# Optimization experiments

Measured on AMD Instinct MI355X. Metric: run time of the kernel, lower is better.

Reference implementation:

```python
import jax, jax.numpy as jnp
import numpy as np
import math

BN_EPS = 1e-5
LOG20 = math.log(20.0)

def conv1x1(w, x):
    # w: [O, C], x: [B, C, N] -> [B, O, N]
    return jnp.einsum('oc,bcn->bon', w, x)

def bn_silu(x, g, b, m, v):
    # inference-mode BatchNorm1d over channel dim, then SiLU
    y = (x - m[None, :, None]) * (g / jnp.sqrt(v + BN_EPS))[None, :, None] + b[None, :, None]
    return y * jax.nn.sigmoid(y)

def setup_inputs() -> dict:
    key = jax.random.key(0)
    ks = jax.random.split(key, 16)
    B, N, M = 8, 4096, 4096
    f32 = jnp.float32
    d = {
        'pcd_f': jax.random.normal(ks[0], (B, 1152, N), f32),
        'img_f': jax.random.normal(ks[1], (B, 1024, M), f32),
        'q_w': jax.random.normal(ks[2], (1024, 1152), f32) * 0.02,
        'k_w': jax.random.normal(ks[3], (1024, 1024), f32) * 0.02,
        'v_w': jax.random.normal(ks[4], (1024, 1024), f32) * 0.02,
        'skip_w': jax.random.normal(ks[5], (1024, 1152), f32) * 0.02,
        'c1_w': jax.random.normal(ks[6], (256, 1024), f32) * 0.03,
        'bn1_g': jnp.ones((256,), f32),
        'bn1_b': jnp.zeros((256,), f32),
        'bn1_m': jax.random.normal(ks[7], (256,), f32) * 0.1,
        'bn1_v': jnp.ones((256,), f32) + 0.1 * jax.random.uniform(ks[8], (256,)),
        'c2_w': jax.random.normal(ks[9], (64, 256), f32) * 0.06,
        'bn2_g': jnp.ones((64,), f32),
        'bn2_b': jnp.zeros((64,), f32),
        'bn2_m': jax.random.normal(ks[10], (64,), f32) * 0.1,
        'bn2_v': jnp.ones((64,), f32) + 0.1 * jax.random.uniform(ks[11], (64,)),
        'c3_w': jax.random.normal(ks[12], (1, 64), f32) * 0.1,
        'c3_b': jnp.zeros((1,), f32),
    }
    return d

def reference(pcd_f, img_f, q_w, k_w, v_w, skip_w, c1_w, bn1_g, bn1_b, bn1_m, bn1_v,
              c2_w, bn2_g, bn2_b, bn2_m, bn2_v, c3_w, c3_b):
    q = conv1x1(q_w, pcd_f)                       # [B, 1024, N]
    k = conv1x1(k_w, img_f)                       # [B, 1024, M]
    v = conv1x1(v_w, img_f)                       # [B, 1024, M]
    scale = math.sqrt(q.shape[1])                 # sqrt(C) = 32
    energy = jnp.einsum('bcn,bcm->bnm', q, k) / scale
    attn = jax.nn.softmax(energy, axis=-1)        # [B, N, M]
    x = jnp.einsum('bnm,bcm->bcn', attn, v)       # [B, 1024, N]
    x = conv1x1(skip_w, pcd_f) + x
    x = bn_silu(conv1x1(c1_w, x), bn1_g, bn1_b, bn1_m, bn1_v)   # [B, 256, N]
    x = bn_silu(conv1x1(c2_w, x), bn2_g, bn2_b, bn2_m, bn2_v)   # [B, 64, N]
    x = conv1x1(c3_w, x) + c3_b[None, :, None]    # [B, 1, N]
    x = x[:, 0, :]                                # squeeze channel -> [B, N]
    return jax.nn.sigmoid(x * LOG20)              # 1/(1+20^-x)
```

## Files before the change

kernel.cpp:

```cpp
#include <hip/hip_runtime.h>

#define LOG20F 2.9957322735539909f
#define AS1 __attribute__((address_space(1)))
#define AS3 __attribute__((address_space(3)))

typedef __attribute__((ext_vector_type(4))) short short4v;
typedef __attribute__((ext_vector_type(8))) short short8;
typedef __attribute__((ext_vector_type(8))) __bf16 bf16x8;
typedef __attribute__((ext_vector_type(4))) float f32x4;

__device__ __forceinline__ short f2bf(float f) {
  unsigned u = __float_as_uint(f);
  u = u + 0x7fffu + ((u >> 16) & 1u);
  return (short)(u >> 16);
}
__device__ __forceinline__ float bf2f(short s) {
  return __uint_as_float(((unsigned)(unsigned short)s) << 16);
}

__device__ __forceinline__ void xcd_map(int& bx, int& by, int& bz) {
  int gx = gridDim.x, gy = gridDim.y;
  int nwg = gx * gy * (int)gridDim.z;
  int lin = bx + gx * (by + gy * bz);
  int q = nwg >> 3, r = nwg & 7;
  int xcd = lin & 7, idx = lin >> 3;
  int wg = (xcd < r ? xcd * (q + 1) : r * (q + 1) + (xcd - r) * q) + idx;
  int per_z = gx * gy;
  bz = wg / per_z;
  int rz = wg - bz * per_z;
  if ((gx & 3) == 0 && (gy & 3) == 0) {
    int nstx = gx >> 2;
    int st = rz >> 4, w = rz & 15;
    bx = ((st % nstx) << 2) + (w & 3);
    by = ((st / nstx) << 2) + (w >> 2);
  } else {
    bx = rz % gx;
    by = rz / gx;
  }
}

template <int EPI>
__global__ __launch_bounds__(512, 2) void gemm8(
    const short* __restrict__ A, const short* __restrict__ B,
    short* __restrict__ C, const short* __restrict__ addp,
    int K, int lda, int ldb, int ldc,
    long abatch, long bbatch, long cbatch, float scale)
{
  __shared__ __align__(16) short lA[2][256 * 64];
  __shared__ __align__(16) short lB[2][256 * 64];

  int bx = blockIdx.x, by = blockIdx.y, bz = blockIdx.z;
  xcd_map(bx, by, bz);

  const int tid = threadIdx.x;
  const int lane = tid & 63, wid = tid >> 6;
  const int wr = wid >> 2, wc = wid & 3;

  const long bm = (long)bx * 256, bn = (long)by * 256;
  const short* Ab = A + (long)bz * abatch + bm * lda;
  const short* Bb = B + (long)bz * bbatch + bn * ldb;

  f32x4 acc[8][4] = {};

  const int NKT = K >> 6;

  auto stageA = [&](int buf, int kt, int half) {
    int k0 = kt << 6;
#pragma unroll
    for (int i = 0; i < 2; ++i) {
      int idx = i * 512 + tid;
      int rl = idx >> 3, ch = idx & 7;
      int row = half * 128 + rl;
      int chs = ch ^ (row & 7);
      __builtin_amdgcn_global_load_lds(
          (const AS1 void*)(Ab + (long)row * lda + k0 + chs * 8),
          (AS3 void*)(&lA[buf][row * 64 + ch * 8]), 16, 0, 0);
    }
  };
  auto stageB = [&](int buf, int kt, int half) {
    int k0 = kt << 6;
#pragma unroll
    for (int i = 0; i < 2; ++i) {
      int idx = i * 512 + tid;
      int rl = idx >> 3, ch = idx & 7;
      int row = half * 128 + rl;
      int chs = ch ^ (row & 7);
      __builtin_amdgcn_global_load_lds(
          (const AS1 void*)(Bb + (long)row * ldb + k0 + chs * 8),
          (AS3 void*)(&lB[buf][row * 64 + ch * 8]), 16, 0, 0);
    }
  };

  const int rr = lane & 15, cl = lane >> 4;
  bf16x8 bfr[4][2], af[2][2];

  auto loadA = [&](int buf, int q) {
#pragma unroll
    for (int f = 0; f < 2; ++f) {
      int row = wr * 128 + q * 32 + f * 16 + rr;
#pragma unroll
      for (int kk = 0; kk < 2; ++kk) {
        int pch = (kk * 4 + cl) ^ (row & 7);
        af[f][kk] = *(const bf16x8*)&lA[buf][row * 64 + pch * 8];
      }
    }
  };
  auto loadB = [&](int buf) {
#pragma unroll
    for (int ni = 0; ni < 4; ++ni) {
      int row = wc * 64 + ni * 16 + rr;
#pragma unroll
      for (int kk = 0; kk < 2; ++kk) {
        int pch = (kk * 4 + cl) ^ (row & 7);
        bfr[ni][kk] = *(const bf16x8*)&lB[buf][row * 64 + pch * 8];
      }
    }
  };

#define BAR() __builtin_amdgcn_s_barrier()
#define LGKM0() asm volatile("s_waitcnt lgkmcnt(0)" ::: "memory")
#define MFMA_Q(q)                                                        \
  do {                                                                   \
    __builtin_amdgcn_s_setprio(1);                                       \
    _Pragma("unroll")                                                    \
    for (int f = 0; f < 2; ++f)                                          \
      _Pragma("unroll")                                                  \
      for (int ni = 0; ni < 4; ++ni)                                     \
        _Pragma("unroll")                                                \
        for (int kk = 0; kk < 2; ++kk)                                   \
          acc[(q) * 2 + f][ni] = __builtin_amdgcn_mfma_f32_16x16x32_bf16(\
              af[f][kk], bfr[ni][kk], acc[(q) * 2 + f][ni], 0, 0, 0);    \
    __builtin_amdgcn_s_setprio(0);                                       \
  } while (0)

  stageB(0, 0, 0); stageB(0, 0, 1);
  stageA(0, 0, 0); stageA(0, 0, 1);
  stageB(1, 1, 0); stageB(1, 1, 1);
  asm volatile("s_waitcnt vmcnt(4)" ::: "memory");
  BAR();

  for (int t2 = 0; t2 < NKT; t2 += 2) {
    const bool more = (t2 + 4 <= NKT);
    loadB(0); loadA(0, 0);
    stageA(1, t2 + 1, 0); stageA(1, t2 + 1, 1);
    BAR(); LGKM0(); MFMA_Q(0); BAR();
    loadA(0, 1);
    if (more) stageB(0, t2 + 2, 0);
    BAR(); LGKM0(); MFMA_Q(1); BAR();
    loadA(0, 2);
    if (more) stageB(0, t2 + 2, 1);
    BAR(); LGKM0(); MFMA_Q(2); BAR();
    loadA(0, 3);
    if (more) { asm volatile("s_waitcnt vmcnt(4)" ::: "memory"); }
    else      { asm volatile("s_waitcnt vmcnt(0)" ::: "memory"); }
    BAR(); LGKM0(); MFMA_Q(3); BAR();
    loadB(1); loadA(1, 0);
    if (more) stageA(0, t2 + 2, 0);
    BAR(); LGKM0(); MFMA_Q(0); BAR();
    loadA(1, 1);
    if (more) stageA(0, t2 + 2, 1);
    BAR(); LGKM0(); MFMA_Q(1); BAR();
    loadA(1, 2);
    if (more) stageB(1, t2 + 3, 0);
    BAR(); LGKM0(); MFMA_Q(2); BAR();
    loadA(1, 3);
    if (more) stageB(1, t2 + 3, 1);
    if (more) { asm volatile("s_waitcnt vmcnt(4)" ::: "memory"); }
    else      { asm volatile("s_waitcnt vmcnt(0)" ::: "memory"); }
    BAR(); LGKM0(); MFMA_Q(3); BAR();
  }
#undef BAR
#undef LGKM0
#undef MFMA_Q

#pragma unroll
  for (int mi = 0; mi < 8; ++mi) {
    long row0 = bm + wr * 128 + (mi >> 1) * 32 + (mi & 1) * 16 + (cl << 2);
#pragma unroll
    for (int ni = 0; ni < 4; ++ni) {
      long col = bn + wc * 64 + ni * 16 + rr;
#pragma unroll
      for (int r = 0; r < 4; ++r) {
        long off = (long)bz * cbatch + (row0 + r) * ldc + col;
        float v = acc[mi][ni][r] * scale;
        if constexpr (EPI == 1) v += bf2f(addp[off]);
        C[off] = f2bf(v);
      }
    }
  }
}

__device__ __forceinline__ int swz32(int row, int ch) {
  return row * 32 + ((ch ^ ((row >> 1) & 3)) << 3);
}

template <int BM, int BN, int WR, int WC, int EPI>
__global__ __launch_bounds__(WR * WC * 64, 4) void gemm_bt(
    const short* __restrict__ A, const short* __restrict__ B,
    short* __restrict__ C, const short* __restrict__ addp,
    const float* __restrict__ sc, const float* __restrict__ sh,
    int K, int lda, int ldb, int ldc,
    long abatch, long bbatch, long cbatch, float scale)
{
  constexpr int NTH = WR * WC * 64;
  constexpr int WM = BM / WR, WN = BN / WC;
  constexpr int MR = WM / 16, NR = WN / 16;
  constexpr int CA = (BM * 4) / NTH, CB = (BN * 4) / NTH;

  __shared__ __align__(16) short lA[2][BM * 32];
  __shared__ __align__(16) short lB[2][BN * 32];

  int bx = blockIdx.x, by = blockIdx.y, bz = blockIdx.z;
  xcd_map(bx, by, bz);

  const int tid = threadIdx.x;
  const int lane = tid & 63, wid = tid >> 6;
  const int wr = wid / WC, wc = wid % WC;

  const long bm = (long)bx * BM, bn = (long)by * BN;
  const short* Ab = A + (long)bz * abatch + bm * lda;
  const short* Bb = B + (long)bz * bbatch + bn * ldb;

  f32x4 acc[MR][NR] = {};

  auto stage = [&](int buf, int k0) {
#pragma unroll
    for (int i = 0; i < CA; ++i) {
      int idx = i * NTH + tid, row = idx >> 2, ch = idx & 3;
      int chs = ch ^ ((row >> 1) & 3);
      __builtin_amdgcn_global_load_lds(
          (const AS1 void*)(Ab + (long)row * lda + k0 + chs * 8),
          (AS3 void*)(&lA[buf][idx * 8]), 16, 0, 0);
    }
#pragma unroll
    for (int i = 0; i < CB; ++i) {
      int idx = i * NTH + tid, row = idx >> 2, ch = idx & 3;
      int chs = ch ^ ((row >> 1) & 3);
      __builtin_amdgcn_global_load_lds(
          (const AS1 void*)(Bb + (long)row * ldb + k0 + chs * 8),
          (AS3 void*)(&lB[buf][idx * 8]), 16, 0, 0);
    }
  };

  const int NT = K >> 5;
  stage(0, 0);
  __syncthreads();
  int cur = 0;
  for (int t = 0; t < NT; ++t) {
    if (t + 1 < NT) stage(cur ^ 1, (t + 1) << 5);
    const int ch = lane >> 4, rrow = lane & 15;
    bf16x8 af[MR], bfr[NR];
#pragma unroll
    for (int mi = 0; mi < MR; ++mi) {
      int row = wr * WM + mi * 16 + rrow;
      af[mi] = *(const bf16x8*)&lA[cur][swz32(row, ch)];
    }
#pragma unroll
    for (int ni = 0; ni < NR; ++ni) {
      int row = wc * WN + ni * 16 + rrow;
      bfr[ni] = *(const bf16x8*)&lB[cur][swz32(row, ch)];
    }
    __builtin_amdgcn_s_setprio(1);
#pragma unroll
    for (int mi = 0; mi < MR; ++mi)
#pragma unroll
      for (int ni = 0; ni < NR; ++ni)
        acc[mi][ni] = __builtin_amdgcn_mfma_f32_16x16x32_bf16(
            af[mi], bfr[ni], acc[mi][ni], 0, 0, 0);
    __builtin_amdgcn_s_setprio(0);
    __syncthreads();
    cur ^= 1;
  }

#pragma unroll
  for (int mi = 0; mi < MR; ++mi) {
    long row0 = bm + wr * WM + mi * 16 + ((lane >> 4) << 2);
#pragma unroll
    for (int ni = 0; ni < NR; ++ni) {
      long col = bn + wc * WN + ni * 16 + (lane & 15);
#pragma unroll
      for (int r = 0; r < 4; ++r) {
        long off = (long)bz * cbatch + (row0 + r) * ldc + col;
        float v = acc[mi][ni][r] * scale;
        if constexpr (EPI == 1) v += bf2f(addp[off]);
        if constexpr (EPI == 2) {
          float y = v * sc[col] + sh[col];
          v = y / (1.f + __expf(-y));
        }
        C[off] = f2bf(v);
      }
    }
  }
}

__global__ __launch_bounds__(256) void transpose_cvt(
    const float* __restrict__ in, short* __restrict__ out, int C, int N)
{
  __shared__ float tile[32][33];
  int n0 = blockIdx.x * 32, c0 = blockIdx.y * 32;
  long z = (long)blockIdx.z * C * N;
  int tx = threadIdx.x & 31, ty = threadIdx.x >> 5;
#pragma unroll
  for (int r = 0; r < 4; ++r) {
    int cc = ty + r * 8;
    tile[cc][tx] = in[z + (long)(c0 + cc) * N + n0 + tx];
  }
  __syncthreads();
#pragma unroll
  for (int r = 0; r < 4; ++r) {
    int nn = ty + r * 8;
    out[z + (long)(n0 + nn) * C + c0 + tx] = f2bf(tile[tx][nn]);
  }
}

__global__ __launch_bounds__(256) void cvt_bf16(
    const float* __restrict__ in, short* __restrict__ out, long n)
{
  long i = ((long)blockIdx.x * 256 + threadIdx.x) * 4;
  if (i >= n) return;
  const float* p = in + i;
  short4v s;
  s[0] = f2bf(p[0]); s[1] = f2bf(p[1]); s[2] = f2bf(p[2]); s[3] = f2bf(p[3]);
  *(short4v*)(out + i) = s;
}

__global__ void bn_prep(const float* g1, const float* b1, const float* m1, const float* v1,
                        const float* g2, const float* b2, const float* m2, const float* v2,
                        float* s1, float* t1, float* s2, float* t2)
{
  int i = threadIdx.x;
  if (i < 256) { float s = g1[i] * rsqrtf(v1[i] + 1e-5f); s1[i] = s; t1[i] = b1[i] - m1[i] * s; }
  if (i < 64)  { float s = g2[i] * rsqrtf(v2[i] + 1e-5f); s2[i] = s; t2[i] = b2[i] - m2[i] * s; }
}

__global__ __launch_bounds__(256) void softmax_row(short* __restrict__ a)
{
  __shared__ float rm[4], rs[4];
  long row = blockIdx.x;
  short* p = a + row * 4096;
  int tid = threadIdx.x;
  short8 v0 = *(short8*)(p + tid * 16);
  short8 v1 = *(short8*)(p + tid * 16 + 8);
  float f[16];
#pragma unroll
  for (int j = 0; j < 8; ++j) { f[j] = bf2f(v0[j]); f[8 + j] = bf2f(v1[j]); }
  float m = f[0];
#pragma unroll
  for (int j = 1; j < 16; ++j) m = fmaxf(m, f[j]);
  for (int o = 32; o > 0; o >>= 1) m = fmaxf(m, __shfl_xor(m, o));
  if ((tid & 63) == 0) rm[tid >> 6] = m;
  __syncthreads();
  m = fmaxf(fmaxf(rm[0], rm[1]), fmaxf(rm[2], rm[3]));
  float s = 0.f;
#pragma unroll
  for (int j = 0; j < 16; ++j) { f[j] = __expf(f[j] - m); s += f[j]; }
  for (int o = 32; o > 0; o >>= 1) s += __shfl_xor(s, o);
  if ((tid & 63) == 0) rs[tid >> 6] = s;
  __syncthreads();
  s = rs[0] + rs[1] + rs[2] + rs[3];
  float inv = 1.f / s;
#pragma unroll
  for (int j = 0; j < 8; ++j) { v0[j] = f2bf(f[j] * inv); v1[j] = f2bf(f[8 + j] * inv); }
  *(short8*)(p + tid * 16) = v0;
  *(short8*)(p + tid * 16 + 8) = v1;
}

__global__ __launch_bounds__(256) void c3_out(
    const short* __restrict__ y2, const float* __restrict__ w,
    const float* __restrict__ bias, float* __restrict__ o, int total)
{
  int i = blockIdx.x * 256 + threadIdx.x;
  if (i >= total) return;
  const short8* r = (const short8*)(y2 + (long)i * 64);
  float acc = 0.f;
#pragma unroll
  for (int j0 = 0; j0 < 8; ++j0) {
    short8 v = r[j0];
#pragma unroll
    for (int j = 0; j < 8; ++j) acc += bf2f(v[j]) * w[j0 * 8 + j];
  }
  acc += bias[0];
  float x = acc * LOG20F;
  o[i] = 1.f / (1.f + __expf(-x));
}

extern "C" void kernel_launch(void* const* d_in, const int* in_sizes, int n_in,
                              void* d_out, int out_size, void* d_ws, size_t ws_size,
                              hipStream_t stream) {
  const float* pcd  = (const float*)d_in[0];
  const float* img  = (const float*)d_in[1];
  const float* qw   = (const float*)d_in[2];
  const float* kw   = (const float*)d_in[3];
  const float* vw   = (const float*)d_in[4];
  const float* skw  = (const float*)d_in[5];
  const float* c1w  = (const float*)d_in[6];
  const float* bn1g = (const float*)d_in[7];
  const float* bn1b = (const float*)d_in[8];
  const float* bn1m = (const float*)d_in[9];
  const float* bn1v = (const float*)d_in[10];
  const float* c2w  = (const float*)d_in[11];
  const float* bn2g = (const float*)d_in[12];
  const float* bn2b = (const float*)d_in[13];
  const float* bn2m = (const float*)d_in[14];
  const float* bn2v = (const float*)d_in[15];
  const float* c3w  = (const float*)d_in[16];
  const float* c3b  = (const float*)d_in[17];
  float* out = (float*)d_out;

  char* ws = (char*)d_ws;
  const long QS = 4096L * 1024;
  const long ES = 4096L * 4096;
  const size_t ALGN = 256;
  auto align_up = [&](size_t x) { return (x + ALGN - 1) & ~(ALGN - 1); };

  size_t oPcd = 0;
  size_t oImg = align_up(oPcd + 8L * 4096 * 1152 * 2);
  size_t oQt  = align_up(oImg + 8L * 4096 * 1024 * 2);
  size_t oKt  = align_up(oQt  + 8L * QS * 2);
  size_t oV   = align_up(oKt  + 8L * QS * 2);
  size_t oSk  = align_up(oV   + 8L * QS * 2);
  size_t oW   = align_up(oSk  + 8L * QS * 2);
  size_t oWq  = oW;
  size_t oWk  = align_up(oWq + 1024L * 1152 * 2);
  size_t oWv  = align_up(oWk + 1024L * 1024 * 2);
  size_t oWs  = align_up(oWv + 1024L * 1024 * 2);
  size_t oC1  = align_up(oWs + 1024L * 1152 * 2);
  size_t oC2  = align_up(oC1 + 256L * 1024 * 2);
  size_t oS1  = align_up(oC2 + 64L * 256 * 2);
  size_t oT1  = align_up(oS1 + 256 * 4);
  size_t oS2  = align_up(oT1 + 256 * 4);
  size_t oT2  = align_up(oS2 + 64 * 4);
  size_t oEnd = align_up(oT2 + 64 * 4);

  short* pcdT  = (short*)(ws + oPcd);
  short* imgT  = (short*)(ws + oImg);
  short* qt    = (short*)(ws + oQt);
  short* kt    = (short*)(ws + oKt);
  short* vbuf  = (short*)(ws + oV);
  short* skipT = (short*)(ws + oSk);
  short* wqb   = (short*)(ws + oWq);
  short* wkb   = (short*)(ws + oWk);
  short* wvb   = (short*)(ws + oWv);
  short* wskb  = (short*)(ws + oWs);
  short* c1b   = (short*)(ws + oC1);
  short* c2b   = (short*)(ws + oC2);
  float* s1 = (float*)(ws + oS1); float* t1 = (float*)(ws + oT1);
  float* s2 = (float*)(ws + oS2); float* t2 = (float*)(ws + oT2);

  int NB; short *attn, *xt;
  if (ws_size >= oEnd + (size_t)(4L * ES * 2)) {
    NB = 4; attn = (short*)(ws + 0); xt = (short*)(ws + oEnd);
  } else {
    NB = 2; attn = imgT; xt = pcdT;
  }
  short* y1t = qt;
  short* y2t = kt;

  cvt_bf16<<<dim3(1152), 256, 0, stream>>>(qw,  wqb,  1024L * 1152);
  cvt_bf16<<<dim3(1024), 256, 0, stream>>>(kw,  wkb,  1024L * 1024);
  cvt_bf16<<<dim3(1024), 256, 0, stream>>>(vw,  wvb,  1024L * 1024);
  cvt_bf16<<<dim3(1152), 256, 0, stream>>>(skw, wskb, 1024L * 1152);
  cvt_bf16<<<dim3(256),  256, 0, stream>>>(c1w, c1b,  256L * 1024);
  cvt_bf16<<<dim3(16),   256, 0, stream>>>(c2w, c2b,  64L * 256);
  bn_prep<<<1, 256, 0, stream>>>(bn1g, bn1b, bn1m, bn1v, bn2g, bn2b, bn2m, bn2v,
                                 s1, t1, s2, t2);
  transpose_cvt<<<dim3(128, 36, 8), 256, 0, stream>>>(pcd, pcdT, 1152, 4096);
  transpose_cvt<<<dim3(128, 32, 8), 256, 0, stream>>>(img, imgT, 1024, 4096);

  gemm8<0><<<dim3(16, 4, 8), 512, 0, stream>>>(
      pcdT, wqb, qt, nullptr, 1152, 1152, 1152, 1024, 4096L * 1152, 0, QS, 1.f);
  gemm8<0><<<dim3(16, 4, 8), 512, 0, stream>>>(
      imgT, wkb, kt, nullptr, 1024, 1024, 1024, 1024, QS, 0, QS, 1.f);
  gemm8<0><<<dim3(4, 16, 8), 512, 0, stream>>>(
      wvb, imgT, vbuf, nullptr, 1024, 1024, 1024, 4096, 0, QS, QS, 1.f);
  gemm8<0><<<dim3(16, 4, 8), 512, 0, stream>>>(
      pcdT, wskb, skipT, nullptr, 1152, 1152, 1152, 1024, 4096L * 1152, 0, QS, 1.f);

  for (int b0 = 0; b0 < 8; b0 += NB) {
    gemm8<0><<<dim3(16, 16, NB), 512, 0, stream>>>(
        qt + (long)b0 * QS, kt + (long)b0 * QS, attn, nullptr,
        1024, 1024, 1024, 4096, QS, QS, ES, 0.03125f);
    softmax_row<<<dim3(4096 * NB), 256, 0, stream>>>(attn);
    gemm8<1><<<dim3(16, 4, NB), 512, 0, stream>>>(
        attn, vbuf + (long)b0 * QS, xt + (long)b0 * QS, skipT + (long)b0 * QS,
        4096, 4096, 4096, 1024, ES, QS, QS, 1.f);
  }

  gemm_bt<128, 128, 2, 2, 2><<<dim3(32, 2, 8), 256, 0, stream>>>(
      xt, c1b, y1t, nullptr, s1, t1,
      1024, 1024, 1024, 256, QS, 0, 4096L * 256, 1.f);
  gemm_bt<128, 64, 4, 1, 2><<<dim3(32, 1, 8), 256, 0, stream>>>(
      y1t, c2b, y2t, nullptr, s2, t2,
      256, 256, 256, 64, 4096L * 256, 0, 4096L * 64, 1.f);
  c3_out<<<dim3(128), 256, 0, stream>>>(y2t, c3w, c3b, out, 32768);

  (void)in_sizes; (void)n_in; (void)out_size; (void)ws_size;
}
```

Measured before the change: 1.143 ms.

## Fuse Q and skip projections, coarsen gemm8 pipeline stages, allow full-batch attention

```diff
diff --git a/kernel.cpp b/kernel.cpp
--- a/kernel.cpp
+++ b/kernel.cpp
@@ -43,8 +43,8 @@
 __global__ __launch_bounds__(512, 2) void gemm8(
     const short* __restrict__ A, const short* __restrict__ B,
     short* __restrict__ C, const short* __restrict__ addp,
-    int K, int lda, int ldb, int ldc,
-    long abatch, long bbatch, long cbatch, float scale)
+    int K, int lda, int ldb, int ldc, int ldadd,
+    long abatch, long bbatch, long cbatch, long addbatch, float scale)
 {
   __shared__ __align__(16) short lA[2][256 * 64];
   __shared__ __align__(16) short lB[2][256 * 64];
@@ -64,26 +64,24 @@
 
   const int NKT = K >> 6;
 
-  auto stageA = [&](int buf, int kt, int half) {
+  auto stageA = [&](int buf, int kt) {
     int k0 = kt << 6;
 #pragma unroll
-    for (int i = 0; i < 2; ++i) {
+    for (int i = 0; i < 4; ++i) {
       int idx = i * 512 + tid;
-      int rl = idx >> 3, ch = idx & 7;
-      int row = half * 128 + rl;
+      int row = idx >> 3, ch = idx & 7;
       int chs = ch ^ (row & 7);
       __builtin_amdgcn_global_load_lds(
           (const AS1 void*)(Ab + (long)row * lda + k0 + chs * 8),
           (AS3 void*)(&lA[buf][row * 64 + ch * 8]), 16, 0, 0);
     }
   };
-  auto stageB = [&](int buf, int kt, int half) {
+  auto stageB = [&](int buf, int kt) {
     int k0 = kt << 6;
 #pragma unroll
-    for (int i = 0; i < 2; ++i) {
+    for (int i = 0; i < 4; ++i) {
       int idx = i * 512 + tid;
-      int rl = idx >> 3, ch = idx & 7;
-      int row = half * 128 + rl;
+      int row = idx >> 3, ch = idx & 7;
       int chs = ch ^ (row & 7);
       __builtin_amdgcn_global_load_lds(
           (const AS1 void*)(Bb + (long)row * ldb + k0 + chs * 8),
@@ -92,12 +90,12 @@
   };
 
   const int rr = lane & 15, cl = lane >> 4;
-  bf16x8 bfr[4][2], af[2][2];
-
-  auto loadA = [&](int buf, int q) {
-#pragma unroll
-    for (int f = 0; f < 2; ++f) {
-      int row = wr * 128 + q * 32 + f * 16 + rr;
+  bf16x8 bfr[4][2], af[4][2];
+
+  auto loadA2 = [&](int buf, int h) {
+#pragma unroll
+    for (int f = 0; f < 4; ++f) {
+      int row = wr * 128 + h * 64 + f * 16 + rr;
 #pragma unroll
       for (int kk = 0; kk < 2; ++kk) {
         int pch = (kk * 4 + cl) ^ (row & 7);
@@ -105,7 +103,7 @@
       }
     }
   };
-  auto loadB = [&](int buf) {
+  auto loadB2 = [&](int buf) {
 #pragma unroll
     for (int ni = 0; ni < 4; ++ni) {
       int row = wc * 64 + ni * 16 + rr;
@@ -119,63 +117,50 @@
 
 #define BAR() __builtin_amdgcn_s_barrier()
 #define LGKM0() asm volatile("s_waitcnt lgkmcnt(0)" ::: "memory")
-#define MFMA_Q(q)                                                        \
+#define MFMA_H(h)                                                        \
   do {                                                                   \
     __builtin_amdgcn_s_setprio(1);                                       \
     _Pragma("unroll")                                                    \
-    for (int f = 0; f < 2; ++f)                                          \
+    for (int f = 0; f < 4; ++f)                                          \
       _Pragma("unroll")                                                  \
       for (int ni = 0; ni < 4; ++ni)                                     \
         _Pragma("unroll")                                                \
         for (int kk = 0; kk < 2; ++kk)                                   \
-          acc[(q) * 2 + f][ni] = __builtin_amdgcn_mfma_f32_16x16x32_bf16(\
-              af[f][kk], bfr[ni][kk], acc[(q) * 2 + f][ni], 0, 0, 0);    \
+          acc[(h) * 4 + f][ni] = __builtin_amdgcn_mfma_f32_16x16x32_bf16(\
+              af[f][kk], bfr[ni][kk], acc[(h) * 4 + f][ni], 0, 0, 0);    \
     __builtin_amdgcn_s_setprio(0);                                       \
   } while (0)
 
-  stageB(0, 0, 0); stageB(0, 0, 1);
-  stageA(0, 0, 0); stageA(0, 0, 1);
-  stageB(1, 1, 0); stageB(1, 1, 1);
+  stageB(0, 0); stageA(0, 0); stageB(1, 1);
   asm volatile("s_waitcnt vmcnt(4)" ::: "memory");
   BAR();
 
   for (int t2 = 0; t2 < NKT; t2 += 2) {
-    const bool more = (t2 + 4 <= NKT);
-    loadB(0); loadA(0, 0);
-    stageA(1, t2 + 1, 0); stageA(1, t2 + 1, 1);
-    BAR(); LGKM0(); MFMA_Q(0); BAR();
-    loadA(0, 1);
-    if (more) stageB(0, t2 + 2, 0);
-    BAR(); LGKM0(); MFMA_Q(1); BAR();
-    loadA(0, 2);
-    if (more) stageB(0, t2 + 2, 1);
-    BAR(); LGKM0(); MFMA_Q(2); BAR();
-    loadA(0, 3);
+    const bool more = (t2 + 2 < NKT);
+    stageA(1, t2 + 1);
+    loadB2(0); loadA2(0, 0);
+    BAR(); LGKM0(); MFMA_H(0); BAR();
+    if (more) stageB(0, t2 + 2);
+    loadA2(0, 1);
     if (more) { asm volatile("s_waitcnt vmcnt(4)" ::: "memory"); }
     else      { asm volatile("s_waitcnt vmcnt(0)" ::: "memory"); }
-    BAR(); LGKM0(); MFMA_Q(3); BAR();
-    loadB(1); loadA(1, 0);
-    if (more) stageA(0, t2 + 2, 0);
-    BAR(); LGKM0(); MFMA_Q(0); BAR();
-    loadA(1, 1);
-    if (more) stageA(0, t2 + 2, 1);
-    BAR(); LGKM0(); MFMA_Q(1); BAR();
-    loadA(1, 2);
-    if (more) stageB(1, t2 + 3, 0);
-    BAR(); LGKM0(); MFMA_Q(2); BAR();
-    loadA(1, 3);
-    if (more) stageB(1, t2 + 3, 1);
+    BAR(); LGKM0(); MFMA_H(1); BAR();
+    if (more) stageA(0, t2 + 2);
+    loadB2(1); loadA2(1, 0);
+    BAR(); LGKM0(); MFMA_H(0); BAR();
+    if (more) stageB(1, t2 + 3);
+    loadA2(1, 1);
     if (more) { asm volatile("s_waitcnt vmcnt(4)" ::: "memory"); }
     else      { asm volatile("s_waitcnt vmcnt(0)" ::: "memory"); }
-    BAR(); LGKM0(); MFMA_Q(3); BAR();
+    BAR(); LGKM0(); MFMA_H(1); BAR();
   }
 #undef BAR
 #undef LGKM0
-#undef MFMA_Q
+#undef MFMA_H
 
 #pragma unroll
   for (int mi = 0; mi < 8; ++mi) {
-    long row0 = bm + wr * 128 + (mi >> 1) * 32 + (mi & 1) * 16 + (cl << 2);
+    long row0 = bm + wr * 128 + (mi >> 2) * 64 + (mi & 3) * 16 + (cl << 2);
 #pragma unroll
     for (int ni = 0; ni < 4; ++ni) {
       long col = bn + wc * 64 + ni * 16 + rr;
@@ -183,7 +168,8 @@
       for (int r = 0; r < 4; ++r) {
         long off = (long)bz * cbatch + (row0 + r) * ldc + col;
         float v = acc[mi][ni][r] * scale;
-        if constexpr (EPI == 1) v += bf2f(addp[off]);
+        if constexpr (EPI == 1)
+          v += bf2f(addp[(long)bz * addbatch + (row0 + r) * ldadd + col]);
         C[off] = f2bf(v);
       }
     }
@@ -408,58 +394,56 @@
   float* out = (float*)d_out;
 
   char* ws = (char*)d_ws;
-  const long QS = 4096L * 1024;
-  const long ES = 4096L * 4096;
+  const long QS  = 4096L * 1024;
+  const long QS2 = 4096L * 2048;
+  const long ES  = 4096L * 4096;
   const size_t ALGN = 256;
   auto align_up = [&](size_t x) { return (x + ALGN - 1) & ~(ALGN - 1); };
 
-  size_t oPcd = 0;
-  size_t oImg = align_up(oPcd + 8L * 4096 * 1152 * 2);
-  size_t oQt  = align_up(oImg + 8L * 4096 * 1024 * 2);
-  size_t oKt  = align_up(oQt  + 8L * QS * 2);
-  size_t oV   = align_up(oKt  + 8L * QS * 2);
-  size_t oSk  = align_up(oV   + 8L * QS * 2);
-  size_t oW   = align_up(oSk  + 8L * QS * 2);
-  size_t oWq  = oW;
-  size_t oWk  = align_up(oWq + 1024L * 1152 * 2);
-  size_t oWv  = align_up(oWk + 1024L * 1024 * 2);
-  size_t oWs  = align_up(oWv + 1024L * 1024 * 2);
-  size_t oC1  = align_up(oWs + 1024L * 1152 * 2);
-  size_t oC2  = align_up(oC1 + 256L * 1024 * 2);
-  size_t oS1  = align_up(oC2 + 64L * 256 * 2);
-  size_t oT1  = align_up(oS1 + 256 * 4);
-  size_t oS2  = align_up(oT1 + 256 * 4);
-  size_t oT2  = align_up(oS2 + 64 * 4);
-  size_t oEnd = align_up(oT2 + 64 * 4);
+  size_t oPcd  = 0;
+  size_t oImg  = align_up(oPcd + 8L * 4096 * 1152 * 2);
+  size_t oQsk  = align_up(oImg + 8L * 4096 * 1024 * 2);
+  size_t oKt   = align_up(oQsk + 8L * QS2 * 2);
+  size_t oV    = align_up(oKt  + 8L * QS * 2);
+  size_t oWqs  = align_up(oV   + 8L * QS * 2);
+  size_t oWk   = align_up(oWqs + 2048L * 1152 * 2);
+  size_t oWv   = align_up(oWk + 1024L * 1024 * 2);
+  size_t oC1   = align_up(oWv + 1024L * 1024 * 2);
+  size_t oC2   = align_up(oC1 + 256L * 1024 * 2);
+  size_t oS1   = align_up(oC2 + 64L * 256 * 2);
+  size_t oT1   = align_up(oS1 + 256 * 4);
+  size_t oS2   = align_up(oT1 + 256 * 4);
+  size_t oT2   = align_up(oS2 + 64 * 4);
+  size_t oEnd  = align_up(oT2 + 64 * 4);
 
   short* pcdT  = (short*)(ws + oPcd);
   short* imgT  = (short*)(ws + oImg);
-  short* qt    = (short*)(ws + oQt);
+  short* qsk   = (short*)(ws + oQsk);
   short* kt    = (short*)(ws + oKt);
   short* vbuf  = (short*)(ws + oV);
-  short* skipT = (short*)(ws + oSk);
-  short* wqb   = (short*)(ws + oWq);
+  short* wqsk  = (short*)(ws + oWqs);
   short* wkb   = (short*)(ws + oWk);
   short* wvb   = (short*)(ws + oWv);
-  short* wskb  = (short*)(ws + oWs);
   short* c1b   = (short*)(ws + oC1);
   short* c2b   = (short*)(ws + oC2);
   float* s1 = (float*)(ws + oS1); float* t1 = (float*)(ws + oT1);
   float* s2 = (float*)(ws + oS2); float* t2 = (float*)(ws + oT2);
 
   int NB; short *attn, *xt;
-  if (ws_size >= oEnd + (size_t)(4L * ES * 2)) {
+  if (ws_size >= oEnd + (size_t)(8L * ES * 2) + (size_t)(8L * QS * 2)) {
+    NB = 8; attn = (short*)(ws + oEnd); xt = (short*)(ws + align_up(oEnd + 8L * ES * 2));
+  } else if (ws_size >= oEnd + (size_t)(8L * QS * 2)) {
     NB = 4; attn = (short*)(ws + 0); xt = (short*)(ws + oEnd);
   } else {
     NB = 2; attn = imgT; xt = pcdT;
   }
-  short* y1t = qt;
+  short* y1t = qsk;
   short* y2t = kt;
 
-  cvt_bf16<<<dim3(1152), 256, 0, stream>>>(qw,  wqb,  1024L * 1152);
+  cvt_bf16<<<dim3(1152), 256, 0, stream>>>(qw,  wqsk,                 1024L * 1152);
+  cvt_bf16<<<dim3(1152), 256, 0, stream>>>(skw, wqsk + 1024L * 1152,  1024L * 1152);
   cvt_bf16<<<dim3(1024), 256, 0, stream>>>(kw,  wkb,  1024L * 1024);
   cvt_bf16<<<dim3(1024), 256, 0, stream>>>(vw,  wvb,  1024L * 1024);
-  cvt_bf16<<<dim3(1152), 256, 0, stream>>>(skw, wskb, 1024L * 1152);
   cvt_bf16<<<dim3(256),  256, 0, stream>>>(c1w, c1b,  256L * 1024);
   cvt_bf16<<<dim3(16),   256, 0, stream>>>(c2w, c2b,  64L * 256);
   bn_prep<<<1, 256, 0, stream>>>(bn1g, bn1b, bn1m, bn1v, bn2g, bn2b, bn2m, bn2v,
@@ -467,23 +451,25 @@
   transpose_cvt<<<dim3(128, 36, 8), 256, 0, stream>>>(pcd, pcdT, 1152, 4096);
   transpose_cvt<<<dim3(128, 32, 8), 256, 0, stream>>>(img, imgT, 1024, 4096);
 
+  gemm8<0><<<dim3(16, 8, 8), 512, 0, stream>>>(
+      pcdT, wqsk, qsk, nullptr,
+      1152, 1152, 1152, 2048, 0, 4096L * 1152, 0, QS2, 0, 1.f);
   gemm8<0><<<dim3(16, 4, 8), 512, 0, stream>>>(
-      pcdT, wqb, qt, nullptr, 1152, 1152, 1152, 1024, 4096L * 1152, 0, QS, 1.f);
-  gemm8<0><<<dim3(16, 4, 8), 512, 0, stream>>>(
-      imgT, wkb, kt, nullptr, 1024, 1024, 1024, 1024, QS, 0, QS, 1.f);
+      imgT, wkb, kt, nullptr,
+      1024, 1024, 1024, 1024, 0, QS, 0, QS, 0, 1.f);
   gemm8<0><<<dim3(4, 16, 8), 512, 0, stream>>>(
-      wvb, imgT, vbuf, nullptr, 1024, 1024, 1024, 4096, 0, QS, QS, 1.f);
-  gemm8<0><<<dim3(16, 4, 8), 512, 0, stream>>>(
-      pcdT, wskb, skipT, nullptr, 1152, 1152, 1152, 1024, 4096L * 1152, 0, QS, 1.f);
+      wvb, imgT, vbuf, nullptr,
+      1024, 1024, 1024, 4096, 0, 0, QS, QS, 0, 1.f);
 
   for (int b0 = 0; b0 < 8; b0 += NB) {
     gemm8<0><<<dim3(16, 16, NB), 512, 0, stream>>>(
-        qt + (long)b0 * QS, kt + (long)b0 * QS, attn, nullptr,
-        1024, 1024, 1024, 4096, QS, QS, ES, 0.03125f);
+        qsk + (long)b0 * QS2, kt + (long)b0 * QS, attn, nullptr,
+        1024, 2048, 1024, 4096, 0, QS2, QS, ES, 0, 0.03125f);
     softmax_row<<<dim3(4096 * NB), 256, 0, stream>>>(attn);
     gemm8<1><<<dim3(16, 4, NB), 512, 0, stream>>>(
-        attn, vbuf + (long)b0 * QS, xt + (long)b0 * QS, skipT + (long)b0 * QS,
-        4096, 4096, 4096, 1024, ES, QS, QS, 1.f);
+        attn, vbuf + (long)b0 * QS, xt + (long)b0 * QS,
+        qsk + (long)b0 * QS2 + 1024,
+        4096, 4096, 4096, 1024, 2048, ES, QS, QS, QS2, 1.f);
   }
 
   gemm_bt<128, 128, 2, 2, 2><<<dim3(32, 2, 8), 256, 0, stream>>>(
```

New measurement: 1.111 ms. 1.03x faster.
